# Kernel optimization log

Hardware: AMD Instinct MI355X
Metric: run time of the kernel (lower is better)

Reference implementation:

```python
import jax, jax.numpy as jnp
import numpy as np

N_NODES = 50000
N_EDGES = 1600000
IN_FEATS = 256
OUT_FEATS = 64


def setup_inputs() -> dict:
    key = jax.random.key(0)
    k1, k2, k3, k4, k5, k6 = jax.random.split(key, 6)
    feature = jax.random.normal(k1, (N_NODES, IN_FEATS), dtype=jnp.float32)
    src = jax.random.randint(k2, (N_EDGES,), 0, N_NODES, dtype=jnp.int32)
    dst = jax.random.randint(k3, (N_EDGES,), 0, N_NODES, dtype=jnp.int32)
    # parameters (xavier-ish scaling)
    W = jax.random.normal(k4, (OUT_FEATS, IN_FEATS), dtype=jnp.float32) * np.sqrt(2.0 / (IN_FEATS + OUT_FEATS))
    att_w = jax.random.normal(k5, (1, 2 * OUT_FEATS), dtype=jnp.float32) * np.sqrt(2.0 / (2 * OUT_FEATS + 1))
    bias = jax.random.normal(k6, (1, OUT_FEATS), dtype=jnp.float32) * np.sqrt(2.0 / (1 + OUT_FEATS))
    return {"feature": feature, "W": W, "att_w": att_w, "bias": bias, "src": src, "dst": dst}


def reference(feature, W, att_w, bias, src, dst):
    # Wh = linear(feature)   [N, out]
    Wh = feature @ W.T
    # concat([Wh_src, Wh_dst]) @ att_w.T  ==  Wh_src@a_src + Wh_dst@a_dst
    a_src = att_w[0, :OUT_FEATS]
    a_dst = att_w[0, OUT_FEATS:]
    el = Wh @ a_src  # [N]
    er = Wh @ a_dst  # [N]
    e = el[src] + er[dst]  # [E]
    e = jax.nn.leaky_relu(e, negative_slope=0.2)
    # segment softmax over incoming edges of each dst node
    e_max = jax.ops.segment_max(e, dst, num_segments=N_NODES)  # -inf for empty
    e_max = jnp.where(jnp.isfinite(e_max), e_max, 0.0)
    e_exp = jnp.exp(e - e_max[dst])
    denom = jax.ops.segment_sum(e_exp, dst, num_segments=N_NODES)
    alpha = e_exp / jnp.where(denom[dst] > 0, denom[dst], 1.0)  # [E]
    # scatter-weighted sum of source features
    h_new = jax.ops.segment_sum(alpha[:, None] * Wh[src], dst, num_segments=N_NODES)
    # residual + bias + activation
    h_new = h_new + Wh
    h_new = jax.nn.elu(h_new + bias)
    return h_new
```

## Files before the change

### kernel.cpp

```cpp
#include <hip/hip_runtime.h>
#include <hip/hip_bf16.h>
#include <math.h>

#define N_NODES 50000
#define N_EDGES 1600000
#define IN_F 256
#define OUT_F 64

#define NBUCKETS 196
#define CAP 10752
#define GEMM_BLOCKS 782
#define BK_BLOCKS 391
#define EPB 4096

typedef short short8 __attribute__((ext_vector_type(8)));
typedef unsigned short ushort8v __attribute__((ext_vector_type(8)));
typedef float f32x4 __attribute__((ext_vector_type(4)));

__device__ __forceinline__ unsigned short f2bf(float f) {
    union { __hip_bfloat16 h; unsigned short u; } v;
    v.h = __float2bfloat16(f);
    return v.u;
}
__device__ __forceinline__ float bf2f(unsigned u) {
    return __uint_as_float(u << 16);
}

__global__ __launch_bounds__(256) void k_prep(const float* __restrict__ W,
                                              unsigned short* __restrict__ wfrag,
                                              int* __restrict__ cnt) {
    const int tid = threadIdx.x;
    if (blockIdx.x == 0 && tid < NBUCKETS) cnt[tid] = 0;
    int c = blockIdx.x * 256 + tid;
    int ct = c >> 9, kt = (c >> 6) & 7, cl = c & 63;
    int col = ct * 16 + (cl & 15);
    int kb = kt * 32 + 8 * (cl >> 4);
    const float* p = W + col * 256 + kb;
    float4 x = *(const float4*)p;
    float4 y = *(const float4*)(p + 4);
    short8 v;
    v[0] = f2bf(x.x); v[1] = f2bf(x.y); v[2] = f2bf(x.z); v[3] = f2bf(x.w);
    v[4] = f2bf(y.x); v[5] = f2bf(y.y); v[6] = f2bf(y.z); v[7] = f2bf(y.w);
    *(short8*)(wfrag + c * 8) = v;
}

__global__ __launch_bounds__(256) void k_main(const float* __restrict__ feat,
                                              const unsigned short* __restrict__ wfrag,
                                              const float* __restrict__ att_w,
                                              unsigned short* __restrict__ whb,
                                              float* __restrict__ el,
                                              float* __restrict__ er,
                                              const int* __restrict__ src,
                                              const int* __restrict__ dst,
                                              int* __restrict__ cnt,
                                              unsigned* __restrict__ pairs) {
    __shared__ unsigned short wlds[16384];
    const int tid = threadIdx.x;

    if (blockIdx.x >= GEMM_BLOCKS) {
        int* lhist = (int*)wlds;
        int* lcur  = lhist + 256;
        const int bbeg = (blockIdx.x - GEMM_BLOCKS) * EPB;

        unsigned wreg[16];
        #pragma unroll
        for (int j = 0; j < 4; ++j) {
            int e0 = bbeg + j * 1024 + tid * 4;
            if (e0 + 3 < N_EDGES) {
                int4 dv = *(const int4*)(dst + e0);
                int4 sv = *(const int4*)(src + e0);
                wreg[j*4+0] = (unsigned)sv.x | ((unsigned)(dv.x & 255) << 16) | ((unsigned)(dv.x >> 8) << 24);
                wreg[j*4+1] = (unsigned)sv.y | ((unsigned)(dv.y & 255) << 16) | ((unsigned)(dv.y >> 8) << 24);
                wreg[j*4+2] = (unsigned)sv.z | ((unsigned)(dv.z & 255) << 16) | ((unsigned)(dv.z >> 8) << 24);
                wreg[j*4+3] = (unsigned)sv.w | ((unsigned)(dv.w & 255) << 16) | ((unsigned)(dv.w >> 8) << 24);
            } else {
                #pragma unroll
                for (int k = 0; k < 4; ++k) {
                    int e = e0 + k;
                    if (e < N_EDGES) {
                        int d = dst[e];
                        wreg[j*4+k] = (unsigned)src[e] | ((unsigned)(d & 255) << 16) | ((unsigned)(d >> 8) << 24);
                    } else wreg[j*4+k] = 0xFF000000u;
                }
            }
        }
        for (int i = tid; i < NBUCKETS; i += 256) lhist[i] = 0;
        __syncthreads();
        #pragma unroll
        for (int k = 0; k < 16; ++k) {
            unsigned b = wreg[k] >> 24;
            if (b < NBUCKETS) atomicAdd(&lhist[b], 1);
        }
        __syncthreads();
        for (int i = tid; i < NBUCKETS; i += 256) {
            int c = lhist[i];
            lcur[i] = c ? (i * CAP + atomicAdd(&cnt[i], c)) : 0;
        }
        __syncthreads();
        #pragma unroll
        for (int k = 0; k < 16; ++k) {
            unsigned wv = wreg[k];
            unsigned b = wv >> 24;
            if (b < NBUCKETS) {
                int pos = atomicAdd(&lcur[b], 1);
                pairs[pos] = wv & 0x00FFFFFFu;
            }
        }
        return;
    }

    const int l = tid & 63, w = tid >> 6;
    const int l15 = l & 15, lg = l >> 4;
    const int wbase = blockIdx.x * 64 + w * 16;
    int ar = wbase + l15; if (ar > N_NODES - 1) ar = N_NODES - 1;
    const float* fbase = feat + (size_t)ar * IN_F + 8 * lg;

    float4 f[16];
    #pragma unroll
    for (int kt = 0; kt < 8; ++kt) {
        f[2*kt]   = *(const float4*)(fbase + kt * 32);
        f[2*kt+1] = *(const float4*)(fbase + kt * 32 + 4);
    }
    #pragma unroll
    for (int i = 0; i < 8; ++i) {
        int c = tid + 256 * i;
        *(short8*)(&wlds[c * 8]) = *(const short8*)(wfrag + c * 8);
    }
    __builtin_amdgcn_sched_barrier(0);
    __syncthreads();

    f32x4 acc[4];
    #pragma unroll
    for (int ct = 0; ct < 4; ++ct) acc[ct] = (f32x4){0.f, 0.f, 0.f, 0.f};

    #pragma unroll
    for (int kt = 0; kt < 8; ++kt) {
        float4 fa = f[2*kt], fb = f[2*kt+1];
        short8 af;
        af[0] = f2bf(fa.x); af[1] = f2bf(fa.y); af[2] = f2bf(fa.z); af[3] = f2bf(fa.w);
        af[4] = f2bf(fb.x); af[5] = f2bf(fb.y); af[6] = f2bf(fb.z); af[7] = f2bf(fb.w);
        short8 b0 = *(const short8*)(&wlds[((0 * 8 + kt) * 64 + l) * 8]);
        short8 b1 = *(const short8*)(&wlds[((1 * 8 + kt) * 64 + l) * 8]);
        short8 b2 = *(const short8*)(&wlds[((2 * 8 + kt) * 64 + l) * 8]);
        short8 b3 = *(const short8*)(&wlds[((3 * 8 + kt) * 64 + l) * 8]);
        acc[0] = __builtin_amdgcn_mfma_f32_16x16x32_bf16(af, b0, acc[0], 0, 0, 0);
        acc[1] = __builtin_amdgcn_mfma_f32_16x16x32_bf16(af, b1, acc[1], 0, 0, 0);
        acc[2] = __builtin_amdgcn_mfma_f32_16x16x32_bf16(af, b2, acc[2], 0, 0, 0);
        acc[3] = __builtin_amdgcn_mfma_f32_16x16x32_bf16(af, b3, acc[3], 0, 0, 0);
    }

    float asrc[4], adst[4];
    #pragma unroll
    for (int ct = 0; ct < 4; ++ct) {
        asrc[ct] = att_w[ct * 16 + l15];
        adst[ct] = att_w[64 + ct * 16 + l15];
    }
    #pragma unroll
    for (int j = 0; j < 4; ++j) {
        int row = wbase + lg * 4 + j;
        float vs = 0.f, vd = 0.f;
        #pragma unroll
        for (int ct = 0; ct < 4; ++ct) {
            float v = acc[ct][j];
            vs += v * asrc[ct];
            vd += v * adst[ct];
            if (row < N_NODES) whb[(size_t)row * OUT_F + ct * 16 + l15] = f2bf(v);
        }
        vs += __shfl_xor(vs, 1); vd += __shfl_xor(vd, 1);
        vs += __shfl_xor(vs, 2); vd += __shfl_xor(vd, 2);
        vs += __shfl_xor(vs, 4); vd += __shfl_xor(vd, 4);
        vs += __shfl_xor(vs, 8); vd += __shfl_xor(vd, 8);
        if (l15 == 0 && row < N_NODES) { el[row] = vs; er[row] = vd; }
    }
}

__global__ __launch_bounds__(1024) void k_build(const int* __restrict__ cnt,
                                                const unsigned* __restrict__ pairs,
                                                const float* __restrict__ el,
                                                const float* __restrict__ er,
                                                int* __restrict__ offs,
                                                int* __restrict__ oend,
                                                unsigned* __restrict__ csr) {
    __shared__ int lcnt[256], ssc[256], lcur[256];
    __shared__ float ler[256];
    const int b = blockIdx.x;
    const int t = threadIdx.x;
    const int ebeg = b * CAP;
    const int nE = cnt[b];

    if (t < 256) {
        lcnt[t] = 0;
        int node = b * 256 + t;
        ler[t] = (node < N_NODES) ? er[node] : 0.f;
    }
    __syncthreads();
    for (int i = t; i < nE; i += 1024)
        atomicAdd(&lcnt[(pairs[ebeg + i] >> 16) & 255], 1);
    __syncthreads();
    if (t < 256) ssc[t] = (lcnt[t] + 7) & ~7;
    __syncthreads();
    for (int d = 1; d < 256; d <<= 1) {
        int v = 0;
        if (t < 256 && t >= d) v = ssc[t - d];
        __syncthreads();
        if (t < 256) ssc[t] += v;
        __syncthreads();
    }
    if (t < 256) {
        int pc = (lcnt[t] + 7) & ~7;
        int base = ssc[t] - pc;
        lcur[t] = base;
        int node = b * 256 + t;
        if (node < N_NODES) { offs[node] = ebeg + base; oend[node] = ebeg + base + pc; }
        for (int k = lcnt[t]; k < pc; ++k) csr[ebeg + base + k] = 0;
    }
    __syncthreads();
    for (int i = t; i < nE; i += 1024) {
        unsigned v = pairs[ebeg + i];
        int n8 = (v >> 16) & 255;
        int s = v & 0xFFFFu;
        float e = el[s] + ler[n8];
        e = (e > 0.f) ? e : 0.2f * e;
        float p = __expf(e);
        int pos = atomicAdd(&lcur[n8], 1);
        csr[ebeg + pos] = (unsigned)s | ((unsigned)f2bf(p) << 16);
    }
}

__global__ __launch_bounds__(256) void k_aggr(const int* __restrict__ offs,
                                              const int* __restrict__ oend,
                                              const unsigned* __restrict__ csr,
                                              const unsigned short* __restrict__ whb,
                                              const float* __restrict__ bias,
                                              float* __restrict__ out) {
    const int wid = __builtin_amdgcn_readfirstlane(threadIdx.x >> 6);
    const int node = blockIdx.x * 4 + wid;
    const int lane = threadIdx.x & 63;
    const int fg = lane & 7, es = lane >> 3;
    const int beg = offs[node], end = oend[node];

    float acc[8] = {0.f, 0.f, 0.f, 0.f, 0.f, 0.f, 0.f, 0.f};
    float den = 0.f;
    #pragma unroll 2
    for (int j = beg; j < end; j += 8) {
        unsigned e = csr[j + es];
        float p = __uint_as_float(e & 0xFFFF0000u);
        const unsigned short* wp = whb + (size_t)(e & 0xFFFFu) * OUT_F + fg * 8;
        ushort8v wv = *(const ushort8v*)wp;
        den += p;
        #pragma unroll
        for (int i = 0; i < 8; ++i) acc[i] = fmaf(p, bf2f((unsigned)wv[i]), acc[i]);
    }
    #pragma unroll
    for (int i = 0; i < 8; ++i) {
        acc[i] += __shfl_xor(acc[i], 8);
        acc[i] += __shfl_xor(acc[i], 16);
        acc[i] += __shfl_xor(acc[i], 32);
    }
    den += __shfl_xor(den, 8); den += __shfl_xor(den, 16); den += __shfl_xor(den, 32);

    if (es == 0) {
        float inv = (end > beg) ? 1.f / den : 0.f;
        ushort8v wn = *(const ushort8v*)(whb + (size_t)node * OUT_F + fg * 8);
        float4 b0 = *(const float4*)(bias + fg * 8);
        float4 b1 = *(const float4*)(bias + fg * 8 + 4);
        float h[8];
        h[0] = acc[0] * inv + bf2f((unsigned)wn[0]) + b0.x;
        h[1] = acc[1] * inv + bf2f((unsigned)wn[1]) + b0.y;
        h[2] = acc[2] * inv + bf2f((unsigned)wn[2]) + b0.z;
        h[3] = acc[3] * inv + bf2f((unsigned)wn[3]) + b0.w;
        h[4] = acc[4] * inv + bf2f((unsigned)wn[4]) + b1.x;
        h[5] = acc[5] * inv + bf2f((unsigned)wn[5]) + b1.y;
        h[6] = acc[6] * inv + bf2f((unsigned)wn[6]) + b1.z;
        h[7] = acc[7] * inv + bf2f((unsigned)wn[7]) + b1.w;
        #pragma unroll
        for (int i = 0; i < 8; ++i) h[i] = (h[i] > 0.f) ? h[i] : __expf(h[i]) - 1.f;
        float* op = out + (size_t)node * OUT_F + fg * 8;
        *(float4*)op = make_float4(h[0], h[1], h[2], h[3]);
        *(float4*)(op + 4) = make_float4(h[4], h[5], h[6], h[7]);
    }
}

extern "C" void kernel_launch(void* const* d_in, const int* in_sizes, int n_in,
                              void* d_out, int out_size, void* d_ws, size_t ws_size,
                              hipStream_t stream) {
    const float* feat  = (const float*)d_in[0];
    const float* W     = (const float*)d_in[1];
    const float* att_w = (const float*)d_in[2];
    const float* bias  = (const float*)d_in[3];
    const int*   src   = (const int*)d_in[4];
    const int*   dst   = (const int*)d_in[5];
    float* out = (float*)d_out;

    unsigned short* whb = (unsigned short*)d_ws;
    unsigned short* wfrag = whb + 3200000;
    float* el      = (float*)d_ws + 1600000 + 8192;
    float* er      = el + 50048;
    int*   offs    = (int*)(er + 50048);
    int*   oend    = offs + 50048;
    int*   cnt     = oend + 50048;
    unsigned* pairs = (unsigned*)(cnt + 512);
    unsigned* csr   = pairs + NBUCKETS * CAP;

    k_prep<<<8, 256, 0, stream>>>(W, wfrag, cnt);
    k_main<<<GEMM_BLOCKS + BK_BLOCKS, 256, 0, stream>>>(feat, wfrag, att_w, whb, el, er,
                                                        src, dst, cnt, pairs);
    k_build<<<NBUCKETS, 1024, 0, stream>>>(cnt, pairs, el, er, offs, oend, csr);
    k_aggr<<<N_NODES / 4, 256, 0, stream>>>(offs, oend, csr, whb, bias, out);
}
```

Baseline: 81.85 us.

## Split fused bucket+GEMM kernel into separate bucket and GEMM launches

The kernel that ran GEMM blocks and edge-bucketing blocks side by side in one launch is split into two kernels, k_bucket and k_gemm, launched one after the other. Each kernel gets its own register and LDS footprint, so the small bucketing blocks no longer reserve the GEMM's 32 KB shared array. In exchange, the overlap between the memory-bound bucketing and the GEMM is lost, and an extra launch is added.

New measurement: 87.78 us. +7.2%, slower.

```diff
diff --git a/kernel.cpp b/kernel.cpp
--- a/kernel.cpp
+++ b/kernel.cpp
@@ -7,11 +7,11 @@
 #define IN_F 256
 #define OUT_F 64
 
-#define NBUCKETS 196
+#define NB 196
 #define CAP 10752
-#define GEMM_BLOCKS 782
 #define BK_BLOCKS 391
 #define EPB 4096
+#define GEMM_BLOCKS 782
 
 typedef short short8 __attribute__((ext_vector_type(8)));
 typedef unsigned short ushort8v __attribute__((ext_vector_type(8)));
@@ -30,7 +30,7 @@
                                               unsigned short* __restrict__ wfrag,
                                               int* __restrict__ cnt) {
     const int tid = threadIdx.x;
-    if (blockIdx.x == 0 && tid < NBUCKETS) cnt[tid] = 0;
+    if (blockIdx.x == 0 && tid < NB) cnt[tid] = 0;
     int c = blockIdx.x * 256 + tid;
     int ct = c >> 9, kt = (c >> 6) & 7, cl = c & 63;
     int col = ct * 16 + (cl & 15);
@@ -44,71 +44,69 @@
     *(short8*)(wfrag + c * 8) = v;
 }
 
-__global__ __launch_bounds__(256) void k_main(const float* __restrict__ feat,
+__global__ __launch_bounds__(256) void k_bucket(const int* __restrict__ src,
+                                                const int* __restrict__ dst,
+                                                int* __restrict__ cnt,
+                                                unsigned* __restrict__ pairs) {
+    __shared__ int lhist[NB];
+    __shared__ int lcur[NB];
+    const int tid = threadIdx.x;
+    const int bbeg = blockIdx.x * EPB;
+
+    unsigned wreg[16];
+    #pragma unroll
+    for (int j = 0; j < 4; ++j) {
+        int e0 = bbeg + j * 1024 + tid * 4;
+        if (e0 + 3 < N_EDGES) {
+            int4 dv = *(const int4*)(dst + e0);
+            int4 sv = *(const int4*)(src + e0);
+            wreg[j*4+0] = (unsigned)sv.x | ((unsigned)(dv.x & 255) << 16) | ((unsigned)(dv.x >> 8) << 24);
+            wreg[j*4+1] = (unsigned)sv.y | ((unsigned)(dv.y & 255) << 16) | ((unsigned)(dv.y >> 8) << 24);
+            wreg[j*4+2] = (unsigned)sv.z | ((unsigned)(dv.z & 255) << 16) | ((unsigned)(dv.z >> 8) << 24);
+            wreg[j*4+3] = (unsigned)sv.w | ((unsigned)(dv.w & 255) << 16) | ((unsigned)(dv.w >> 8) << 24);
+        } else {
+            #pragma unroll
+            for (int k = 0; k < 4; ++k) {
+                int e = e0 + k;
+                if (e < N_EDGES) {
+                    int d = dst[e];
+                    wreg[j*4+k] = (unsigned)src[e] | ((unsigned)(d & 255) << 16) | ((unsigned)(d >> 8) << 24);
+                } else wreg[j*4+k] = 0xFF000000u;
+            }
+        }
+    }
+    if (tid < NB) lhist[tid] = 0;
+    __syncthreads();
+    #pragma unroll
+    for (int k = 0; k < 16; ++k) {
+        unsigned b = wreg[k] >> 24;
+        if (b < NB) atomicAdd(&lhist[b], 1);
+    }
+    __syncthreads();
+    if (tid < NB) {
+        int c = lhist[tid];
+        lcur[tid] = c ? (tid * CAP + atomicAdd(&cnt[tid], c)) : 0;
+    }
+    __syncthreads();
+    #pragma unroll
+    for (int k = 0; k < 16; ++k) {
+        unsigned wv = wreg[k];
+        unsigned b = wv >> 24;
+        if (b < NB) {
+            int pos = atomicAdd(&lcur[b], 1);
+            pairs[pos] = wv & 0x00FFFFFFu;
+        }
+    }
+}
+
+__global__ __launch_bounds__(256) void k_gemm(const float* __restrict__ feat,
                                               const unsigned short* __restrict__ wfrag,
                                               const float* __restrict__ att_w,
                                               unsigned short* __restrict__ whb,
                                               float* __restrict__ el,
-                                              float* __restrict__ er,
-                                              const int* __restrict__ src,
-                                              const int* __restrict__ dst,
-                                              int* __restrict__ cnt,
-                                              unsigned* __restrict__ pairs) {
+                                              float* __restrict__ er) {
     __shared__ unsigned short wlds[16384];
     const int tid = threadIdx.x;
-
-    if (blockIdx.x >= GEMM_BLOCKS) {
-        int* lhist = (int*)wlds;
-        int* lcur  = lhist + 256;
-        const int bbeg = (blockIdx.x - GEMM_BLOCKS) * EPB;
-
-        unsigned wreg[16];
-        #pragma unroll
-        for (int j = 0; j < 4; ++j) {
-            int e0 = bbeg + j * 1024 + tid * 4;
-            if (e0 + 3 < N_EDGES) {
-                int4 dv = *(const int4*)(dst + e0);
-                int4 sv = *(const int4*)(src + e0);
-                wreg[j*4+0] = (unsigned)sv.x | ((unsigned)(dv.x & 255) << 16) | ((unsigned)(dv.x >> 8) << 24);
-                wreg[j*4+1] = (unsigned)sv.y | ((unsigned)(dv.y & 255) << 16) | ((unsigned)(dv.y >> 8) << 24);
-                wreg[j*4+2] = (unsigned)sv.z | ((unsigned)(dv.z & 255) << 16) | ((unsigned)(dv.z >> 8) << 24);
-                wreg[j*4+3] = (unsigned)sv.w | ((unsigned)(dv.w & 255) << 16) | ((unsigned)(dv.w >> 8) << 24);
-            } else {
-                #pragma unroll
-                for (int k = 0; k < 4; ++k) {
-                    int e = e0 + k;
-                    if (e < N_EDGES) {
-                        int d = dst[e];
-                        wreg[j*4+k] = (unsigned)src[e] | ((unsigned)(d & 255) << 16) | ((unsigned)(d >> 8) << 24);
-                    } else wreg[j*4+k] = 0xFF000000u;
-                }
-            }
-        }
-        for (int i = tid; i < NBUCKETS; i += 256) lhist[i] = 0;
-        __syncthreads();
-        #pragma unroll
-        for (int k = 0; k < 16; ++k) {
-            unsigned b = wreg[k] >> 24;
-            if (b < NBUCKETS) atomicAdd(&lhist[b], 1);
-        }
-        __syncthreads();
-        for (int i = tid; i < NBUCKETS; i += 256) {
-            int c = lhist[i];
-            lcur[i] = c ? (i * CAP + atomicAdd(&cnt[i], c)) : 0;
-        }
-        __syncthreads();
-        #pragma unroll
-        for (int k = 0; k < 16; ++k) {
-            unsigned wv = wreg[k];
-            unsigned b = wv >> 24;
-            if (b < NBUCKETS) {
-                int pos = atomicAdd(&lcur[b], 1);
-                pairs[pos] = wv & 0x00FFFFFFu;
-            }
-        }
-        return;
-    }
-
     const int l = tid & 63, w = tid >> 6;
     const int l15 = l & 15, lg = l >> 4;
     const int wbase = blockIdx.x * 64 + w * 16;
@@ -300,11 +298,11 @@
     int*   oend    = offs + 50048;
     int*   cnt     = oend + 50048;
     unsigned* pairs = (unsigned*)(cnt + 512);
-    unsigned* csr   = pairs + NBUCKETS * CAP;
+    unsigned* csr   = pairs + NB * CAP;
 
     k_prep<<<8, 256, 0, stream>>>(W, wfrag, cnt);
-    k_main<<<GEMM_BLOCKS + BK_BLOCKS, 256, 0, stream>>>(feat, wfrag, att_w, whb, el, er,
-                                                        src, dst, cnt, pairs);
-    k_build<<<NBUCKETS, 1024, 0, stream>>>(cnt, pairs, el, er, offs, oend, csr);
+    k_bucket<<<BK_BLOCKS, 256, 0, stream>>>(src, dst, cnt, pairs);
+    k_gemm<<<GEMM_BLOCKS, 256, 0, stream>>>(feat, wfrag, att_w, whb, el, er);
+    k_build<<<NB, 1024, 0, stream>>>(cnt, pairs, el, er, offs, oend, csr);
     k_aggr<<<N_NODES / 4, 256, 0, stream>>>(offs, oend, csr, whb, bias, out);
 }
```
